# Performance work log

Measured on AMD Instinct MI355X. Metric: run time of the kernel, lower is better.

The kernel has to match this reference:

```python
import jax, jax.numpy as jnp
import numpy as np

WS = (2, 8, 8)      # window size (wt, wh, ww)
SS = (1, 4, 4)      # shift size
HEADS = 6


def _window_partition(x, ws):
    B, T, H, W, C = x.shape
    wt, wh, ww = ws
    x = x.reshape(B, T // wt, wt, H // wh, wh, W // ww, ww, C)
    x = x.transpose(0, 1, 3, 5, 2, 4, 6, 7)
    return x.reshape(-1, wt * wh * ww, C)  # (B*nW, N, C)


def _window_reverse(w, ws, B, T, H, W):
    wt, wh, ww = ws
    C = w.shape[-1]
    x = w.reshape(B, T // wt, H // wh, W // ww, wt, wh, ww, C)
    x = x.transpose(0, 1, 4, 2, 5, 3, 6, 7)
    return x.reshape(B, T, H, W, C)


def _rel_pos_index(ws):
    wt, wh, ww = ws
    coords = np.stack(np.meshgrid(np.arange(wt), np.arange(wh), np.arange(ww), indexing='ij'))
    coords = coords.reshape(3, -1)                      # (3, N)
    rel = coords[:, :, None] - coords[:, None, :]       # (3, N, N)
    rel = rel.transpose(1, 2, 0).astype(np.int32)
    rel[..., 0] += wt - 1
    rel[..., 1] += wh - 1
    rel[..., 2] += ww - 1
    rel[..., 0] *= (2 * wh - 1) * (2 * ww - 1)
    rel[..., 1] *= (2 * ww - 1)
    return rel.sum(-1)                                  # (N, N)


def _shift_mask(T, H, W, ws, ss):
    # standard Swin shifted-window attention mask
    img = np.zeros((1, T, H, W, 1), dtype=np.float32)
    cnt = 0
    for t in (slice(0, -ws[0]), slice(-ws[0], -ss[0]), slice(-ss[0], None)):
        for h in (slice(0, -ws[1]), slice(-ws[1], -ss[1]), slice(-ss[1], None)):
            for w in (slice(0, -ws[2]), slice(-ws[2], -ss[2]), slice(-ss[2], None)):
                img[:, t, h, w, :] = cnt
                cnt += 1
    mw = np.asarray(_window_partition(jnp.asarray(img), ws)).squeeze(-1)  # (nW, N)
    diff = mw[:, None, :] - mw[:, :, None]
    return jnp.asarray(np.where(diff != 0, -100.0, 0.0).astype(np.float32))


def setup_inputs() -> dict:
    key = jax.random.key(0)
    ks = jax.random.split(key, 9)
    B, T, H, W, C = 2, 8, 64, 64, 192
    hid = 4 * C
    s = 0.02
    x = jax.random.normal(ks[0], (B, T, H, W, C), jnp.float32)
    qkv_w = jax.random.normal(ks[1], (3 * C, C), jnp.float32) * s
    qkv_b = jnp.zeros((3 * C,), jnp.float32)
    proj_w = jax.random.normal(ks[2], (C, C), jnp.float32) * s
    proj_b = jnp.zeros((C,), jnp.float32)
    n_rel = (2 * WS[0] - 1) * (2 * WS[1] - 1) * (2 * WS[2] - 1)
    rpb_table = jax.random.normal(ks[3], (n_rel, HEADS), jnp.float32) * s
    rpb_index = jnp.asarray(_rel_pos_index(WS))
    fc1_w = jax.random.normal(ks[4], (hid, C), jnp.float32) * s
    fc1_b = jnp.zeros((hid,), jnp.float32)
    fc2_w = jax.random.normal(ks[5], (C, hid), jnp.float32) * s
    fc2_b = jnp.zeros((C,), jnp.float32)
    attn_mask = _shift_mask(T, H, W, WS, SS)
    return dict(x=x, attn_mask=attn_mask, qkv_w=qkv_w, qkv_b=qkv_b, proj_w=proj_w,
                proj_b=proj_b, rpb_table=rpb_table, rpb_index=rpb_index,
                fc1_w=fc1_w, fc1_b=fc1_b, fc2_w=fc2_w, fc2_b=fc2_b)


def reference(x, attn_mask, qkv_w, qkv_b, proj_w, proj_b, rpb_table, rpb_index,
              fc1_w, fc1_b, fc2_w, fc2_b):
    B, T, H, W, C = x.shape
    h = HEADS
    d = C // h
    scale = d ** -0.5

    shifted = jnp.roll(x, (-SS[0], -SS[1], -SS[2]), axis=(1, 2, 3))
    xw = _window_partition(shifted, WS)            # (Bn, N, C)
    Bn, N, _ = xw.shape

    qkv = (xw @ qkv_w.T + qkv_b).reshape(Bn, N, 3, h, d).transpose(2, 0, 3, 1, 4)
    q, k, v = qkv[0], qkv[1], qkv[2]               # (Bn, h, N, d)
    attn = jnp.einsum('bhnd,bhmd->bhnm', q * scale, k)
    bias = rpb_table[rpb_index.reshape(-1)].reshape(N, N, h).transpose(2, 0, 1)
    attn = attn + bias[None]
    nW = attn_mask.shape[0]
    attn = (attn.reshape(Bn // nW, nW, h, N, N) + attn_mask[None, :, None]).reshape(Bn, h, N, N)
    attn = jax.nn.softmax(attn, axis=-1)
    out = jnp.einsum('bhnm,bhmd->bhnd', attn, v).transpose(0, 2, 1, 3).reshape(Bn, N, C)
    out = out @ proj_w.T + proj_b

    z = _window_reverse(out, WS, B, T, H, W)
    z = jnp.roll(z, (SS[0], SS[1], SS[2]), axis=(1, 2, 3))

    y = z + x
    mlp = jax.nn.gelu(y @ fc1_w.T + fc1_b, approximate=False) @ fc2_w.T + fc2_b
    return x + mlp
```

## Files before the change

kernel.cpp:

```cpp
#include <hip/hip_runtime.h>
#include <hip/hip_bf16.h>

typedef __attribute__((ext_vector_type(4))) float f32x4;
typedef __attribute__((ext_vector_type(8))) short bf16x8;

#define DEV __device__ __forceinline__

DEV unsigned short f2bf(float f) {
  union { float f; unsigned int u; } v; v.f = f;
  unsigned int r = v.u + 0x7fffu + ((v.u >> 16) & 1u);
  return (unsigned short)(r >> 16);
}

DEV float bf2f(unsigned short u) {
  union { unsigned int u; float f; } v; v.u = ((unsigned int)u) << 16; return v.f;
}

DEV short2 pkbf(float a, float b) {
  float2 t; t.x = a; t.y = b;
  __hip_bfloat162 h = __float22bfloat162_rn(t);
  union { __hip_bfloat162 h; short2 s; } u; u.h = h; return u.s;
}

DEV bf16x8 cvt8(float4 u, float4 v) {
  short2 a = pkbf(u.x, u.y), b = pkbf(u.z, u.w), c = pkbf(v.x, v.y), d = pkbf(v.z, v.w);
  bf16x8 r;
  r[0] = a.x; r[1] = a.y; r[2] = b.x; r[3] = b.y;
  r[4] = c.x; r[5] = c.y; r[6] = d.x; r[7] = d.y;
  return r;
}

DEV float gelu_fast(float v) {
  float u = 1.5957691216057308f * v * (1.0f + 0.044715f * v * v);
  return v * __builtin_amdgcn_rcpf(1.0f + __expf(-u));
}

DEV size_t winmap(int row) {
  int wIdx = row >> 7, n = row & 127;
  int b = wIdx >> 8, widx = wIdx & 255;
  int t = (((widx >> 6) * 2 + (n >> 6)) + 1) & 7;
  int h = ((((widx >> 3) & 7) * 8 + ((n >> 3) & 7)) + 4) & 63;
  int w = (((widx & 7) * 8 + (n & 7)) + 4) & 63;
  return (size_t)(((b * 8 + t) * 64 + h) * 64 + w);
}

DEV int reg3(int tw, int hw, int ww, int n) {
  int ts = tw * 2 + (n >> 6);
  int hs = hw * 8 + ((n >> 3) & 7);
  int wsv = ww * 8 + (n & 7);
  int rt = (ts >= 7) ? 2 : ((ts >= 6) ? 1 : 0);
  int rh = (hs >= 60) ? 2 : ((hs >= 56) ? 1 : 0);
  int rw = (wsv >= 60) ? 2 : ((wsv >= 56) ? 1 : 0);
  return rt * 9 + rh * 3 + rw;
}

DEV void gload16(const unsigned short* g, unsigned short* lds) {
  __builtin_amdgcn_global_load_lds(
      (const __attribute__((address_space(1))) unsigned int*)g,
      (__attribute__((address_space(3))) unsigned int*)lds, 16, 0, 0);
}

__global__ __launch_bounds__(256) void k_prep(
    const float* __restrict__ qkv_w, const float* __restrict__ proj_w,
    const float* __restrict__ fc1_w, const float* __restrict__ fc2_w,
    const float* __restrict__ rpb_t, const int* __restrict__ rpb_i,
    unsigned short* __restrict__ wq, unsigned short* __restrict__ wp,
    unsigned short* __restrict__ w1, unsigned short* __restrict__ w2,
    float* __restrict__ b6) {
  int i = blockIdx.x * 256 + threadIdx.x;
  if (i < 110592) wq[i] = f2bf(qkv_w[i]);
  if (i < 36864)  wp[i] = f2bf(proj_w[i]);
  if (i < 147456) { w1[i] = f2bf(fc1_w[i]); w2[i] = f2bf(fc2_w[i]); }
  if (i < 16384) {
    int row = i >> 7, col = i & 127;
    int idx = rpb_i[i];
    int dest = (row >> 4) * 2048 + (((row >> 2) & 3) * 16 + (col & 15)) * 32 +
               (col >> 4) * 4 + (row & 3);
    #pragma unroll
    for (int h = 0; h < 6; ++h) b6[h * 16384 + dest] = rpb_t[idx * 6 + h];
  }
}

__global__ __launch_bounds__(256) void k_qkv(
    const float* __restrict__ x, const unsigned short* __restrict__ Bm,
    const float* __restrict__ bias, unsigned short* __restrict__ outb) {
  __shared__ char smem[40960];
  float* As = (float*)smem;
  unsigned short* Bs = (unsigned short*)(smem + 32768);
  unsigned short* Cs = (unsigned short*)smem;
  const int tid = threadIdx.x;
  const int wave = tid >> 6, lane = tid & 63;
  const int lin = ((int)blockIdx.x & 7) * 576 + ((int)blockIdx.x >> 3);
  const int mt = lin / 9, nt = lin - mt * 9;
  const int m0 = mt * 128, n0 = nt * 64;
  const int wr = wave >> 1, wc = wave & 1;
  const int l8 = lane >> 3, s8 = lane & 7;

  const float* aptr[8];
  #pragma unroll
  for (int i = 0; i < 8; ++i) {
    int row = wave * 32 + i * 4 + (lane >> 4);
    aptr[i] = x + winmap(m0 + row) * 192 + (((lane & 15) ^ (row & 15)) << 2);
  }

  f32x4 acc[4][2] = {};
  for (int kt = 0; kt < 192; kt += 64) {
    __syncthreads();
    #pragma unroll
    for (int i = 0; i < 8; ++i)
      gload16((const unsigned short*)(aptr[i] + kt), (unsigned short*)(As + (wave * 8 + i) * 256));
    #pragma unroll
    for (int j = 0; j < 2; ++j) {
      int c = wave * 2 + j;
      int row = c * 8 + l8;
      gload16(Bm + (size_t)(n0 + row) * 192 + kt + (s8 ^ l8) * 8, Bs + c * 512);
    }
    __syncthreads();

    #pragma unroll
    for (int kk = 0; kk < 2; ++kk) {
      bf16x8 af[4], bfr[2];
      #pragma unroll
      for (int mi = 0; mi < 4; ++mi) {
        int r = wr * 64 + mi * 16 + (lane & 15);
        int s0 = kk * 8 + (lane >> 4) * 2;
        float4 u = *(const float4*)(As + r * 64 + ((s0 ^ (r & 15)) << 2));
        float4 v = *(const float4*)(As + r * 64 + (((s0 + 1) ^ (r & 15)) << 2));
        af[mi] = cvt8(u, v);
      }
      #pragma unroll
      for (int ni = 0; ni < 2; ++ni) {
        int row = wc * 32 + ni * 16 + (lane & 15);
        int slot = (kk * 4 + (lane >> 4)) ^ (row & 7);
        bfr[ni] = *(const bf16x8*)(Bs + row * 64 + slot * 8);
      }
      #pragma unroll
      for (int mi = 0; mi < 4; ++mi)
        #pragma unroll
        for (int ni = 0; ni < 2; ++ni)
          acc[mi][ni] = __builtin_amdgcn_mfma_f32_16x16x32_bf16(af[mi], bfr[ni], acc[mi][ni], 0, 0, 0);
    }
  }

  __syncthreads();
  #pragma unroll
  for (int ni = 0; ni < 2; ++ni) {
    int coll = wc * 32 + ni * 16 + (lane & 15);
    float bb = bias[n0 + coll];
    #pragma unroll
    for (int mi = 0; mi < 4; ++mi) {
      int rbase = wr * 64 + mi * 16 + ((lane >> 4) << 2);
      #pragma unroll
      for (int j = 0; j < 4; ++j)
        Cs[(rbase + j) * 72 + coll] = f2bf(acc[mi][ni][j] + bb);
    }
  }
  __syncthreads();
  const int row = tid >> 1, hh = tid & 1;
  unsigned short* gb = outb + (size_t)(m0 + row) * 576 + n0 + hh * 32;
  #pragma unroll
  for (int s = 0; s < 4; ++s)
    *(bf16x8*)(gb + s * 8) = *(const bf16x8*)(Cs + row * 72 + hh * 32 + s * 8);
}

enum { EPI_BF16 = 0, EPI_PROJ = 2 };

template <int EPI, int GATHER>
__global__ __launch_bounds__(256) void gemm_bt(
    const void* __restrict__ Ap, const unsigned short* __restrict__ Bm,
    const float* __restrict__ bias, unsigned short* __restrict__ outb,
    const float* __restrict__ xres, int N, int K, int NT) {
  __shared__ unsigned short sh[128 * 72];
  unsigned short* Bs = sh;
  const int tid = threadIdx.x;
  const int wave = tid >> 6, lane = tid & 63;
  const int total = (int)gridDim.x;
  const int lin = ((int)blockIdx.x & 7) * (total >> 3) + ((int)blockIdx.x >> 3);
  const int mt = lin / NT, nt = lin - mt * NT;
  const int m0 = mt * 128, n0 = nt * 64;
  const int wr = wave >> 1, wc = wave & 1;
  const int l8 = lane >> 3, s8 = lane & 7;
  const unsigned short* Ab = (const unsigned short*)Ap;

  size_t abase[4];
  #pragma unroll
  for (int mi = 0; mi < 4; ++mi) {
    int arow = m0 + wr * 64 + mi * 16 + (lane & 15);
    abase[mi] = (size_t)arow * K;
  }

  f32x4 acc[4][2] = {};
  for (int kt = 0; kt < K; kt += 64) {
    __syncthreads();
    #pragma unroll
    for (int i = 0; i < 2; ++i) {
      int c = wave * 2 + i;
      int row = c * 8 + l8;
      gload16(Bm + (size_t)(n0 + row) * K + kt + (s8 ^ l8) * 8, Bs + c * 512);
    }
    __syncthreads();

    #pragma unroll
    for (int kk = 0; kk < 2; ++kk) {
      bf16x8 af[4], bfr[2];
      #pragma unroll
      for (int mi = 0; mi < 4; ++mi)
        af[mi] = *(const bf16x8*)(Ab + abase[mi] + kt + kk * 32 + (lane >> 4) * 8);
      #pragma unroll
      for (int ni = 0; ni < 2; ++ni) {
        int row = wc * 32 + ni * 16 + (lane & 15);
        int slot = (kk * 4 + (lane >> 4)) ^ (row & 7);
        bfr[ni] = *(const bf16x8*)(Bs + row * 64 + slot * 8);
      }
      #pragma unroll
      for (int mi = 0; mi < 4; ++mi)
        #pragma unroll
        for (int ni = 0; ni < 2; ++ni)
          acc[mi][ni] = __builtin_amdgcn_mfma_f32_16x16x32_bf16(af[mi], bfr[ni], acc[mi][ni], 0, 0, 0);
    }
  }

  __syncthreads();
  #pragma unroll
  for (int ni = 0; ni < 2; ++ni) {
    int coll = wc * 32 + ni * 16 + (lane & 15);
    float bb = bias[n0 + coll];
    #pragma unroll
    for (int mi = 0; mi < 4; ++mi) {
      int rbase = wr * 64 + mi * 16 + ((lane >> 4) << 2);
      #pragma unroll
      for (int j = 0; j < 4; ++j)
        sh[(rbase + j) * 72 + coll] = f2bf(acc[mi][ni][j] + bb);
    }
  }
  __syncthreads();
  const int row = tid >> 1, hh = tid & 1;
  if (EPI == EPI_BF16) {
    unsigned short* gb = outb + (size_t)(m0 + row) * N + n0 + hh * 32;
    #pragma unroll
    for (int s = 0; s < 4; ++s)
      *(bf16x8*)(gb + s * 8) = *(const bf16x8*)(sh + row * 72 + hh * 32 + s * 8);
  } else {
    size_t gf = winmap(m0 + row) * 192 + n0 + hh * 32;
    #pragma unroll
    for (int s = 0; s < 4; ++s) {
      bf16x8 cv = *(const bf16x8*)(sh + row * 72 + hh * 32 + s * 8);
      float4 x0 = *(const float4*)(xres + gf + s * 8);
      float4 x1 = *(const float4*)(xres + gf + s * 8 + 4);
      bf16x8 o;
      o[0] = (short)f2bf(bf2f((unsigned short)cv[0]) + x0.x);
      o[1] = (short)f2bf(bf2f((unsigned short)cv[1]) + x0.y);
      o[2] = (short)f2bf(bf2f((unsigned short)cv[2]) + x0.z);
      o[3] = (short)f2bf(bf2f((unsigned short)cv[3]) + x0.w);
      o[4] = (short)f2bf(bf2f((unsigned short)cv[4]) + x1.x);
      o[5] = (short)f2bf(bf2f((unsigned short)cv[5]) + x1.y);
      o[6] = (short)f2bf(bf2f((unsigned short)cv[6]) + x1.z);
      o[7] = (short)f2bf(bf2f((unsigned short)cv[7]) + x1.w);
      *(bf16x8*)(outb + gf + s * 8) = o;
    }
  }
}

__global__ __launch_bounds__(256) void k_attn(const unsigned short* __restrict__ qkv,
                                              const float* __restrict__ bias6,
                                              unsigned short* __restrict__ attn_out) {
  __shared__ unsigned short Kl[128 * 32];
  __shared__ unsigned short Vt[32 * 136];
  __shared__ unsigned short Pl[128 * 140];
  const int lin = ((int)blockIdx.x & 7) * 384 + ((int)blockIdx.x >> 3);
  const int wIdx = lin / 6;
  const int hd = lin - wIdx * 6;
  const int tid = threadIdx.x;
  const int wave = tid >> 6, lane = tid & 63;
  const int lrow = lane & 15, lk = lane >> 4;
  const int widx = wIdx & 255;
  const int tw = widx >> 6, hw = (widx >> 3) & 7, ww = widx & 7;
  const size_t qbase = (size_t)wIdx * 73728;

  #pragma unroll
  for (int r = 0; r < 2; ++r) {
    int idx = r * 256 + tid;
    int row = idx >> 2, slot = idx & 3;
    int m = (row + (row >> 2)) & 3;
    *(bf16x8*)(Kl + row * 32 + ((slot ^ m) * 8)) =
        *(const bf16x8*)(qkv + qbase + (size_t)row * 576 + 192 + hd * 32 + slot * 8);
  }
  {
    int vtok = tid & 127, shalf = tid >> 7;
    #pragma unroll
    for (int so = 0; so < 2; ++so) {
      int slot = shalf * 2 + so;
      bf16x8 v = *(const bf16x8*)(qkv + qbase + (size_t)vtok * 576 + 384 + hd * 32 + slot * 8);
      #pragma unroll
      for (int j = 0; j < 8; ++j)
        Vt[(slot * 8 + j) * 136 + vtok] = (unsigned short)v[j];
    }
  }
  bf16x8 qf[2];
  #pragma unroll
  for (int tr = 0; tr < 2; ++tr)
    qf[tr] = *(const bf16x8*)(qkv + qbase +
                              (size_t)(wave * 32 + tr * 16 + lrow) * 576 +
                              hd * 32 + lk * 8);
  int rcol[8];
  #pragma unroll
  for (int tc = 0; tc < 8; ++tc) rcol[tc] = reg3(tw, hw, ww, tc * 16 + lrow);
  __syncthreads();

  f32x4 s[2][8];
  #pragma unroll
  for (int tc = 0; tc < 8; ++tc) {
    int krow = tc * 16 + lrow;
    int m = (krow + (krow >> 2)) & 3;
    bf16x8 kf = *(const bf16x8*)(Kl + krow * 32 + ((lk ^ m) * 8));
    #pragma unroll
    for (int tr = 0; tr < 2; ++tr) {
      f32x4 z = {0.f, 0.f, 0.f, 0.f};
      s[tr][tc] = __builtin_amdgcn_mfma_f32_16x16x32_bf16(qf[tr], kf, z, 0, 0, 0);
    }
  }

  const float scale = 0.17677669529663687f;
  #pragma unroll
  for (int tr = 0; tr < 2; ++tr) {
    int rb = wave * 2 + tr;
    const float* bp = bias6 + hd * 16384 + rb * 2048 + lane * 32;
    f32x4 bb[8];
    #pragma unroll
    for (int tc = 0; tc < 8; ++tc) bb[tc] = *(const f32x4*)(bp + tc * 4);
    int rreg[4];
    #pragma unroll
    for (int j = 0; j < 4; ++j) rreg[j] = reg3(tw, hw, ww, rb * 16 + lk * 4 + j);
    #pragma unroll
    for (int tc = 0; tc < 8; ++tc) {
      #pragma unroll
      for (int j = 0; j < 4; ++j) {
        float v = fmaf(s[tr][tc][j], scale,
                       bb[tc][j] + ((rreg[j] == rcol[tc]) ? 0.0f : -100.0f));
        int row = rb * 16 + lk * 4 + j;
        Pl[row * 140 + tc * 16 + lrow] = f2bf(__expf(v));
      }
    }
  }
  __syncthreads();

  bf16x8 ones;
  #pragma unroll
  for (int j = 0; j < 8; ++j) ones[j] = (short)0x3F80;
  f32x4 o[2][2] = {};
  f32x4 osum[2] = {};
  #pragma unroll
  for (int ks = 0; ks < 4; ++ks) {
    bf16x8 pa[2], vb[2];
    #pragma unroll
    for (int tr = 0; tr < 2; ++tr)
      pa[tr] = *(const bf16x8*)(Pl + (wave * 32 + tr * 16 + lrow) * 140 +
                                ks * 32 + lk * 8);
    #pragma unroll
    for (int nc = 0; nc < 2; ++nc)
      vb[nc] = *(const bf16x8*)(Vt + (nc * 16 + lrow) * 136 + ks * 32 + lk * 8);
    #pragma unroll
    for (int tr = 0; tr < 2; ++tr) {
      #pragma unroll
      for (int nc = 0; nc < 2; ++nc)
        o[tr][nc] = __builtin_amdgcn_mfma_f32_16x16x32_bf16(pa[tr], vb[nc], o[tr][nc], 0, 0, 0);
      osum[tr] = __builtin_amdgcn_mfma_f32_16x16x32_bf16(pa[tr], ones, osum[tr], 0, 0, 0);
    }
  }

  #pragma unroll
  for (int tr = 0; tr < 2; ++tr) {
    #pragma unroll
    for (int j = 0; j < 4; ++j) {
      float rinv = __builtin_amdgcn_rcpf(osum[tr][j]);
      int row = wave * 32 + tr * 16 + lk * 4 + j;
      #pragma unroll
      for (int nc = 0; nc < 2; ++nc) {
        attn_out[((size_t)wIdx * 128 + row) * 192 + hd * 32 + nc * 16 + lrow] =
            f2bf(o[tr][nc][j] * rinv);
      }
    }
  }
}

DEV void stage_w(const unsigned short* w1, const unsigned short* w2, int hb,
                 char* smem, int buf, int wave, int lane) {
  unsigned short* d1 = (unsigned short*)(smem + buf * 12288);
  unsigned short* d2 = (unsigned short*)(smem + 24576 + buf * 12288);
  const int l8 = lane >> 3, s8 = lane & 7;
  {
    int c = wave, p = c >> 2, q = c & 3;
    gload16(w1 + (size_t)(hb + q * 8 + l8) * 192 + p * 64 + ((s8 ^ l8) * 8), d1 + c * 512);
  }
  if (wave < 4) {
    int c = 8 + wave, p = c >> 2, q = c & 3;
    gload16(w1 + (size_t)(hb + q * 8 + l8) * 192 + p * 64 + ((s8 ^ l8) * 8), d1 + c * 512);
  }
  {
    int c = wave;
    int rg = c * 16 + (lane >> 2);
    gload16(w2 + (size_t)rg * 768 + hb + (((lane & 3) ^ ((rg >> 1) & 3)) * 8), d2 + c * 512);
  }
  if (wave < 4) {
    int c = 8 + wave;
    int rg = c * 16 + (lane >> 2);
    gload16(w2 + (size_t)rg * 768 + hb + (((lane & 3) ^ ((rg >> 1) & 3)) * 8), d2 + c * 512);
  }
}

__global__ __launch_bounds__(512, 4) void k_mlp(
    const unsigned short* __restrict__ y, const unsigned short* __restrict__ w1,
    const float* __restrict__ b1, const unsigned short* __restrict__ w2,
    const float* __restrict__ b2, const float* __restrict__ xin,
    float* __restrict__ out) {
  __shared__ char smem[57344];
  unsigned short* Hs = (unsigned short*)(smem + 49152);
  const int tid = threadIdx.x;
  const int wave = tid >> 6, lane = tid & 63;
  const int lrow = lane & 15, lk = lane >> 4;
  const int m0 = (int)blockIdx.x * 128;
  const int tok = wave * 16 + lrow;
  const int tq = (lrow >> 1) & 3;

  bf16x8 yfr[6];
  {
    const unsigned short* yp = y + (size_t)(m0 + tok) * 192 + lk * 8;
    #pragma unroll
    for (int kk = 0; kk < 6; ++kk) yfr[kk] = *(const bf16x8*)(yp + kk * 32);
  }

  stage_w(w1, w2, 0, smem, 0, wave, lane);
  stage_w(w1, w2, 32, smem, 1, wave, lane);
  __syncthreads();

  f32x4 oacc[12] = {};
  for (int c = 0; c < 24; ++c) {
    const int hb = c * 32;
    unsigned short* w1b = (unsigned short*)(smem + (c & 1) * 12288);
    unsigned short* w2b = (unsigned short*)(smem + 24576 + (c & 1) * 12288);

    f32x4 hacc[2] = {};
    #pragma unroll
    for (int kk = 0; kk < 6; ++kk) {
      int p = kk >> 1, sc = (kk & 1) * 4;
      #pragma unroll
      for (int hi = 0; hi < 2; ++hi) {
        bf16x8 av = *(const bf16x8*)(w1b + p * 2048 + (hi * 16 + lrow) * 64 +
                                     (((sc + lk) ^ (lrow & 7)) * 8));
        hacc[hi] = __builtin_amdgcn_mfma_f32_16x16x32_bf16(av, yfr[kk], hacc[hi], 0, 0, 0);
      }
    }

    #pragma unroll
    for (int hi = 0; hi < 2; ++hi) {
      float4 bb = *(const float4*)(b1 + hb + hi * 16 + lk * 4);
      short2 p01 = pkbf(gelu_fast(hacc[hi][0] + bb.x), gelu_fast(hacc[hi][1] + bb.y));
      short2 p23 = pkbf(gelu_fast(hacc[hi][2] + bb.z), gelu_fast(hacc[hi][3] + bb.w));
      ushort4 o;
      o.x = (unsigned short)p01.x; o.y = (unsigned short)p01.y;
      o.z = (unsigned short)p23.x; o.w = (unsigned short)p23.y;
      int g = hi * 4 + lk;
      *(ushort4*)(Hs + tok * 32 + (((g >> 1) ^ tq) * 8) + (g & 1) * 4) = o;
    }

    {
      bf16x8 af = *(const bf16x8*)(Hs + tok * 32 + ((lk ^ tq) * 8));
      #pragma unroll
      for (int ni = 0; ni < 12; ++ni) {
        int n = ni * 16 + lrow;
        bf16x8 bv = *(const bf16x8*)(w2b + n * 32 + ((lk ^ ((n >> 1) & 3)) * 8));
        oacc[ni] = __builtin_amdgcn_mfma_f32_16x16x32_bf16(af, bv, oacc[ni], 0, 0, 0);
      }
    }

    __syncthreads();
    if (c < 22) stage_w(w1, w2, hb + 64, smem, c & 1, wave, lane);
  }

  #pragma unroll
  for (int ni = 0; ni < 12; ++ni) {
    int col = ni * 16 + lrow;
    float bb = b2[col];
    #pragma unroll
    for (int j = 0; j < 4; ++j) {
      size_t idx = (size_t)(m0 + wave * 16 + lk * 4 + j) * 192 + col;
      out[idx] = xin[idx] + oacc[ni][j] + bb;
    }
  }
}

extern "C" void kernel_launch(void* const* d_in, const int* in_sizes, int n_in,
                              void* d_out, int out_size, void* d_ws, size_t ws_size,
                              hipStream_t stream) {
  const float* x      = (const float*)d_in[0];
  const float* qkv_w  = (const float*)d_in[2];
  const float* qkv_b  = (const float*)d_in[3];
  const float* proj_w = (const float*)d_in[4];
  const float* proj_b = (const float*)d_in[5];
  const float* rpb_t  = (const float*)d_in[6];
  const int*   rpb_i  = (const int*)d_in[7];
  const float* fc1_w  = (const float*)d_in[8];
  const float* fc1_b  = (const float*)d_in[9];
  const float* fc2_w  = (const float*)d_in[10];
  const float* fc2_b  = (const float*)d_in[11];
  float* out = (float*)d_out;
  char* ws = (char*)d_ws;

  unsigned short* qkv = (unsigned short*)(ws + 0);
  unsigned short* att = (unsigned short*)(ws + 75497472);
  unsigned short* ybf = (unsigned short*)(ws + 100663296);
  unsigned short* wq  = (unsigned short*)(ws + 125829120);
  unsigned short* wp  = (unsigned short*)(ws + 126050304);
  unsigned short* w1  = (unsigned short*)(ws + 126124032);
  unsigned short* w2  = (unsigned short*)(ws + 126418944);
  float*          b6  = (float*)(ws + 126713856);

  k_prep<<<576, 256, 0, stream>>>(qkv_w, proj_w, fc1_w, fc2_w, rpb_t, rpb_i, wq, wp, w1, w2, b6);
  k_qkv<<<4608, 256, 0, stream>>>(x, wq, qkv_b, qkv);
  k_attn<<<3072, 256, 0, stream>>>(qkv, b6, att);
  gemm_bt<EPI_PROJ, 0><<<1536, 256, 0, stream>>>(att, wp, proj_b, ybf, x, 192, 192, 3);
  k_mlp<<<512, 512, 0, stream>>>(ybf, w1, fc1_b, w2, fc2_b, x, out);
}
```

Before: 183.8 us.

## Fuse window attention with output projection and residual into one kernel

Replaces the separate per-(window, head) attention kernel and the projection GEMM with a single kernel: one 512-thread block per window loops over the six heads and accumulates each head's contribution to the projection in registers. It then adds the bias and the residual and scatters the result to y. This removes the round trip of the attention output through global memory and one kernel launch. In exchange, parallelism drops from 3072 blocks to 512 and each head step is serialized behind several barriers. The final stores are scalar 2-byte writes rather than vectorized ones.

```diff
diff --git a/kernel.cpp b/kernel.cpp
--- a/kernel.cpp
+++ b/kernel.cpp
@@ -163,222 +163,146 @@
     *(bf16x8*)(gb + s * 8) = *(const bf16x8*)(Cs + row * 72 + hh * 32 + s * 8);
 }
 
-enum { EPI_BF16 = 0, EPI_PROJ = 2 };
-
-template <int EPI, int GATHER>
-__global__ __launch_bounds__(256) void gemm_bt(
-    const void* __restrict__ Ap, const unsigned short* __restrict__ Bm,
-    const float* __restrict__ bias, unsigned short* __restrict__ outb,
-    const float* __restrict__ xres, int N, int K, int NT) {
-  __shared__ unsigned short sh[128 * 72];
-  unsigned short* Bs = sh;
-  const int tid = threadIdx.x;
-  const int wave = tid >> 6, lane = tid & 63;
-  const int total = (int)gridDim.x;
-  const int lin = ((int)blockIdx.x & 7) * (total >> 3) + ((int)blockIdx.x >> 3);
-  const int mt = lin / NT, nt = lin - mt * NT;
-  const int m0 = mt * 128, n0 = nt * 64;
-  const int wr = wave >> 1, wc = wave & 1;
-  const int l8 = lane >> 3, s8 = lane & 7;
-  const unsigned short* Ab = (const unsigned short*)Ap;
-
-  size_t abase[4];
-  #pragma unroll
-  for (int mi = 0; mi < 4; ++mi) {
-    int arow = m0 + wr * 64 + mi * 16 + (lane & 15);
-    abase[mi] = (size_t)arow * K;
-  }
-
-  f32x4 acc[4][2] = {};
-  for (int kt = 0; kt < K; kt += 64) {
-    __syncthreads();
-    #pragma unroll
-    for (int i = 0; i < 2; ++i) {
-      int c = wave * 2 + i;
-      int row = c * 8 + l8;
-      gload16(Bm + (size_t)(n0 + row) * K + kt + (s8 ^ l8) * 8, Bs + c * 512);
-    }
-    __syncthreads();
-
-    #pragma unroll
-    for (int kk = 0; kk < 2; ++kk) {
-      bf16x8 af[4], bfr[2];
-      #pragma unroll
-      for (int mi = 0; mi < 4; ++mi)
-        af[mi] = *(const bf16x8*)(Ab + abase[mi] + kt + kk * 32 + (lane >> 4) * 8);
-      #pragma unroll
-      for (int ni = 0; ni < 2; ++ni) {
-        int row = wc * 32 + ni * 16 + (lane & 15);
-        int slot = (kk * 4 + (lane >> 4)) ^ (row & 7);
-        bfr[ni] = *(const bf16x8*)(Bs + row * 64 + slot * 8);
-      }
-      #pragma unroll
-      for (int mi = 0; mi < 4; ++mi)
-        #pragma unroll
-        for (int ni = 0; ni < 2; ++ni)
-          acc[mi][ni] = __builtin_amdgcn_mfma_f32_16x16x32_bf16(af[mi], bfr[ni], acc[mi][ni], 0, 0, 0);
-    }
-  }
-
-  __syncthreads();
-  #pragma unroll
-  for (int ni = 0; ni < 2; ++ni) {
-    int coll = wc * 32 + ni * 16 + (lane & 15);
-    float bb = bias[n0 + coll];
-    #pragma unroll
-    for (int mi = 0; mi < 4; ++mi) {
-      int rbase = wr * 64 + mi * 16 + ((lane >> 4) << 2);
-      #pragma unroll
-      for (int j = 0; j < 4; ++j)
-        sh[(rbase + j) * 72 + coll] = f2bf(acc[mi][ni][j] + bb);
-    }
-  }
-  __syncthreads();
-  const int row = tid >> 1, hh = tid & 1;
-  if (EPI == EPI_BF16) {
-    unsigned short* gb = outb + (size_t)(m0 + row) * N + n0 + hh * 32;
-    #pragma unroll
-    for (int s = 0; s < 4; ++s)
-      *(bf16x8*)(gb + s * 8) = *(const bf16x8*)(sh + row * 72 + hh * 32 + s * 8);
-  } else {
-    size_t gf = winmap(m0 + row) * 192 + n0 + hh * 32;
-    #pragma unroll
-    for (int s = 0; s < 4; ++s) {
-      bf16x8 cv = *(const bf16x8*)(sh + row * 72 + hh * 32 + s * 8);
-      float4 x0 = *(const float4*)(xres + gf + s * 8);
-      float4 x1 = *(const float4*)(xres + gf + s * 8 + 4);
-      bf16x8 o;
-      o[0] = (short)f2bf(bf2f((unsigned short)cv[0]) + x0.x);
-      o[1] = (short)f2bf(bf2f((unsigned short)cv[1]) + x0.y);
-      o[2] = (short)f2bf(bf2f((unsigned short)cv[2]) + x0.z);
-      o[3] = (short)f2bf(bf2f((unsigned short)cv[3]) + x0.w);
-      o[4] = (short)f2bf(bf2f((unsigned short)cv[4]) + x1.x);
-      o[5] = (short)f2bf(bf2f((unsigned short)cv[5]) + x1.y);
-      o[6] = (short)f2bf(bf2f((unsigned short)cv[6]) + x1.z);
-      o[7] = (short)f2bf(bf2f((unsigned short)cv[7]) + x1.w);
-      *(bf16x8*)(outb + gf + s * 8) = o;
-    }
-  }
-}
-
-__global__ __launch_bounds__(256) void k_attn(const unsigned short* __restrict__ qkv,
-                                              const float* __restrict__ bias6,
-                                              unsigned short* __restrict__ attn_out) {
+DEV void stage_head(const unsigned short* qkv, size_t qbase, int h,
+                    const unsigned short* wp, unsigned short* Kl,
+                    unsigned short* Vt, unsigned short* Wp,
+                    int tid, int wave, int lane) {
+  {
+    int row = tid >> 2, slot = tid & 3;
+    int m = (row + (row >> 2)) & 3;
+    *(bf16x8*)(Kl + row * 32 + ((slot ^ m) * 8)) =
+        *(const bf16x8*)(qkv + qbase + (size_t)row * 576 + 192 + h * 32 + slot * 8);
+  }
+  {
+    int vtok = tid & 127, slot = tid >> 7;
+    bf16x8 v = *(const bf16x8*)(qkv + qbase + (size_t)vtok * 576 + 384 + h * 32 + slot * 8);
+    #pragma unroll
+    for (int j = 0; j < 8; ++j) Vt[(slot * 8 + j) * 136 + vtok] = (unsigned short)v[j];
+  }
+  {
+    int c = wave;
+    int rg = c * 16 + (lane >> 2);
+    gload16(wp + (size_t)rg * 192 + h * 32 + (((lane & 3) ^ ((rg >> 1) & 3)) * 8), Wp + c * 512);
+    if (wave < 4) {
+      int c2 = 8 + wave;
+      int rg2 = c2 * 16 + (lane >> 2);
+      gload16(wp + (size_t)rg2 * 192 + h * 32 + (((lane & 3) ^ ((rg2 >> 1) & 3)) * 8), Wp + c2 * 512);
+    }
+  }
+}
+
+__global__ __launch_bounds__(512, 4) void k_attnproj(
+    const unsigned short* __restrict__ qkv, const float* __restrict__ bias6,
+    const unsigned short* __restrict__ wp, const float* __restrict__ proj_b,
+    const float* __restrict__ x, unsigned short* __restrict__ ybf) {
   __shared__ unsigned short Kl[128 * 32];
   __shared__ unsigned short Vt[32 * 136];
   __shared__ unsigned short Pl[128 * 140];
-  const int lin = ((int)blockIdx.x & 7) * 384 + ((int)blockIdx.x >> 3);
-  const int wIdx = lin / 6;
-  const int hd = lin - wIdx * 6;
+  __shared__ unsigned short Os[128 * 40];
+  __shared__ unsigned short Wp[192 * 32];
   const int tid = threadIdx.x;
   const int wave = tid >> 6, lane = tid & 63;
   const int lrow = lane & 15, lk = lane >> 4;
+  const int wIdx = ((int)blockIdx.x & 7) * 64 + ((int)blockIdx.x >> 3);
   const int widx = wIdx & 255;
   const int tw = widx >> 6, hw = (widx >> 3) & 7, ww = widx & 7;
   const size_t qbase = (size_t)wIdx * 73728;
-
-  #pragma unroll
-  for (int r = 0; r < 2; ++r) {
-    int idx = r * 256 + tid;
-    int row = idx >> 2, slot = idx & 3;
-    int m = (row + (row >> 2)) & 3;
-    *(bf16x8*)(Kl + row * 32 + ((slot ^ m) * 8)) =
-        *(const bf16x8*)(qkv + qbase + (size_t)row * 576 + 192 + hd * 32 + slot * 8);
-  }
-  {
-    int vtok = tid & 127, shalf = tid >> 7;
-    #pragma unroll
-    for (int so = 0; so < 2; ++so) {
-      int slot = shalf * 2 + so;
-      bf16x8 v = *(const bf16x8*)(qkv + qbase + (size_t)vtok * 576 + 384 + hd * 32 + slot * 8);
-      #pragma unroll
-      for (int j = 0; j < 8; ++j)
-        Vt[(slot * 8 + j) * 136 + vtok] = (unsigned short)v[j];
-    }
-  }
-  bf16x8 qf[2];
-  #pragma unroll
-  for (int tr = 0; tr < 2; ++tr)
-    qf[tr] = *(const bf16x8*)(qkv + qbase +
-                              (size_t)(wave * 32 + tr * 16 + lrow) * 576 +
-                              hd * 32 + lk * 8);
+  const float scale = 0.17677669529663687f;
+
   int rcol[8];
   #pragma unroll
   for (int tc = 0; tc < 8; ++tc) rcol[tc] = reg3(tw, hw, ww, tc * 16 + lrow);
-  __syncthreads();
-
-  f32x4 s[2][8];
-  #pragma unroll
-  for (int tc = 0; tc < 8; ++tc) {
-    int krow = tc * 16 + lrow;
-    int m = (krow + (krow >> 2)) & 3;
-    bf16x8 kf = *(const bf16x8*)(Kl + krow * 32 + ((lk ^ m) * 8));
-    #pragma unroll
-    for (int tr = 0; tr < 2; ++tr) {
+  int rreg[4];
+  #pragma unroll
+  for (int j = 0; j < 4; ++j) rreg[j] = reg3(tw, hw, ww, wave * 16 + lk * 4 + j);
+
+  bf16x8 ones;
+  #pragma unroll
+  for (int j = 0; j < 8; ++j) ones[j] = (short)0x3F80;
+
+  stage_head(qkv, qbase, 0, wp, Kl, Vt, Wp, tid, wave, lane);
+
+  f32x4 oaccP[12] = {};
+  for (int h = 0; h < 6; ++h) {
+    __syncthreads();
+
+    bf16x8 qf = *(const bf16x8*)(qkv + qbase + (size_t)(wave * 16 + lrow) * 576 +
+                                 h * 32 + lk * 8);
+    f32x4 s[8];
+    #pragma unroll
+    for (int tc = 0; tc < 8; ++tc) {
+      int krow = tc * 16 + lrow;
+      int m = (krow + (krow >> 2)) & 3;
+      bf16x8 kf = *(const bf16x8*)(Kl + krow * 32 + ((lk ^ m) * 8));
       f32x4 z = {0.f, 0.f, 0.f, 0.f};
-      s[tr][tc] = __builtin_amdgcn_mfma_f32_16x16x32_bf16(qf[tr], kf, z, 0, 0, 0);
-    }
-  }
-
-  const float scale = 0.17677669529663687f;
-  #pragma unroll
-  for (int tr = 0; tr < 2; ++tr) {
-    int rb = wave * 2 + tr;
-    const float* bp = bias6 + hd * 16384 + rb * 2048 + lane * 32;
-    f32x4 bb[8];
-    #pragma unroll
-    for (int tc = 0; tc < 8; ++tc) bb[tc] = *(const f32x4*)(bp + tc * 4);
-    int rreg[4];
-    #pragma unroll
-    for (int j = 0; j < 4; ++j) rreg[j] = reg3(tw, hw, ww, rb * 16 + lk * 4 + j);
-    #pragma unroll
-    for (int tc = 0; tc < 8; ++tc) {
-      #pragma unroll
-      for (int j = 0; j < 4; ++j) {
-        float v = fmaf(s[tr][tc][j], scale,
-                       bb[tc][j] + ((rreg[j] == rcol[tc]) ? 0.0f : -100.0f));
-        int row = rb * 16 + lk * 4 + j;
-        Pl[row * 140 + tc * 16 + lrow] = f2bf(__expf(v));
-      }
-    }
-  }
-  __syncthreads();
-
-  bf16x8 ones;
-  #pragma unroll
-  for (int j = 0; j < 8; ++j) ones[j] = (short)0x3F80;
-  f32x4 o[2][2] = {};
-  f32x4 osum[2] = {};
-  #pragma unroll
-  for (int ks = 0; ks < 4; ++ks) {
-    bf16x8 pa[2], vb[2];
-    #pragma unroll
-    for (int tr = 0; tr < 2; ++tr)
-      pa[tr] = *(const bf16x8*)(Pl + (wave * 32 + tr * 16 + lrow) * 140 +
-                                ks * 32 + lk * 8);
-    #pragma unroll
-    for (int nc = 0; nc < 2; ++nc)
-      vb[nc] = *(const bf16x8*)(Vt + (nc * 16 + lrow) * 136 + ks * 32 + lk * 8);
-    #pragma unroll
-    for (int tr = 0; tr < 2; ++tr) {
+      s[tc] = __builtin_amdgcn_mfma_f32_16x16x32_bf16(qf, kf, z, 0, 0, 0);
+    }
+
+    {
+      const float* bp = bias6 + h * 16384 + wave * 2048 + lane * 32;
+      f32x4 bb[8];
+      #pragma unroll
+      for (int tc = 0; tc < 8; ++tc) bb[tc] = *(const f32x4*)(bp + tc * 4);
+      #pragma unroll
+      for (int tc = 0; tc < 8; ++tc) {
+        #pragma unroll
+        for (int j = 0; j < 4; ++j) {
+          float v = fmaf(s[tc][j], scale,
+                         bb[tc][j] + ((rreg[j] == rcol[tc]) ? 0.0f : -100.0f));
+          int row = wave * 16 + lk * 4 + j;
+          Pl[row * 140 + tc * 16 + lrow] = f2bf(__expf(v));
+        }
+      }
+    }
+    __syncthreads();
+
+    f32x4 o[2] = {};
+    f32x4 osum = {};
+    #pragma unroll
+    for (int ks = 0; ks < 4; ++ks) {
+      bf16x8 pa = *(const bf16x8*)(Pl + (wave * 16 + lrow) * 140 + ks * 32 + lk * 8);
+      #pragma unroll
+      for (int nc = 0; nc < 2; ++nc) {
+        bf16x8 vb = *(const bf16x8*)(Vt + (nc * 16 + lrow) * 136 + ks * 32 + lk * 8);
+        o[nc] = __builtin_amdgcn_mfma_f32_16x16x32_bf16(pa, vb, o[nc], 0, 0, 0);
+      }
+      osum = __builtin_amdgcn_mfma_f32_16x16x32_bf16(pa, ones, osum, 0, 0, 0);
+    }
+    #pragma unroll
+    for (int j = 0; j < 4; ++j) {
+      float rinv = __builtin_amdgcn_rcpf(osum[j]);
+      int row = wave * 16 + lk * 4 + j;
       #pragma unroll
       for (int nc = 0; nc < 2; ++nc)
-        o[tr][nc] = __builtin_amdgcn_mfma_f32_16x16x32_bf16(pa[tr], vb[nc], o[tr][nc], 0, 0, 0);
-      osum[tr] = __builtin_amdgcn_mfma_f32_16x16x32_bf16(pa[tr], ones, osum[tr], 0, 0, 0);
-    }
-  }
-
-  #pragma unroll
-  for (int tr = 0; tr < 2; ++tr) {
+        Os[row * 40 + nc * 16 + lrow] = f2bf(o[nc][j] * rinv);
+    }
+    __syncthreads();
+
+    {
+      bf16x8 af = *(const bf16x8*)(Os + (wave * 16 + lrow) * 40 + lk * 8);
+      #pragma unroll
+      for (int ni = 0; ni < 12; ++ni) {
+        int n = ni * 16 + lrow;
+        bf16x8 bv = *(const bf16x8*)(Wp + n * 32 + ((lk ^ ((n >> 1) & 3)) * 8));
+        oaccP[ni] = __builtin_amdgcn_mfma_f32_16x16x32_bf16(af, bv, oaccP[ni], 0, 0, 0);
+      }
+    }
+    __syncthreads();
+    if (h < 5) stage_head(qkv, qbase, h + 1, wp, Kl, Vt, Wp, tid, wave, lane);
+  }
+
+  size_t gf[4];
+  #pragma unroll
+  for (int j = 0; j < 4; ++j)
+    gf[j] = winmap(wIdx * 128 + wave * 16 + lk * 4 + j) * 192;
+  #pragma unroll
+  for (int ni = 0; ni < 12; ++ni) {
+    int col = ni * 16 + lrow;
+    float bb = proj_b[col];
     #pragma unroll
     for (int j = 0; j < 4; ++j) {
-      float rinv = __builtin_amdgcn_rcpf(osum[tr][j]);
-      int row = wave * 32 + tr * 16 + lk * 4 + j;
-      #pragma unroll
-      for (int nc = 0; nc < 2; ++nc) {
-        attn_out[((size_t)wIdx * 128 + row) * 192 + hd * 32 + nc * 16 + lrow] =
-            f2bf(o[tr][nc][j] * rinv);
-      }
+      size_t idx = gf[j] + col;
+      ybf[idx] = f2bf(oaccP[ni][j] + bb + x[idx]);
     }
   }
 }
@@ -507,7 +431,6 @@
   char* ws = (char*)d_ws;
 
   unsigned short* qkv = (unsigned short*)(ws + 0);
-  unsigned short* att = (unsigned short*)(ws + 75497472);
   unsigned short* ybf = (unsigned short*)(ws + 100663296);
   unsigned short* wq  = (unsigned short*)(ws + 125829120);
   unsigned short* wp  = (unsigned short*)(ws + 126050304);
@@ -517,7 +440,6 @@
 
   k_prep<<<576, 256, 0, stream>>>(qkv_w, proj_w, fc1_w, fc2_w, rpb_t, rpb_i, wq, wp, w1, w2, b6);
   k_qkv<<<4608, 256, 0, stream>>>(x, wq, qkv_b, qkv);
-  k_attn<<<3072, 256, 0, stream>>>(qkv, b6, att);
-  gemm_bt<EPI_PROJ, 0><<<1536, 256, 0, stream>>>(att, wp, proj_b, ybf, x, 192, 192, 3);
+  k_attnproj<<<512, 512, 0, stream>>>(qkv, b6, wp, proj_b, x, ybf);
   k_mlp<<<512, 512, 0, stream>>>(ybf, w1, fc1_b, w2, fc2_b, x, out);
 }
```

After: 175.2 us, median of 3. -4.7%, faster.
